# Performance work log

Measured on AMD Instinct MI355X. Metric: run time of the kernel, lower is better.

The kernel has to match this reference:

```python
import jax, jax.numpy as jnp
import numpy as np

B, S, E, F = 8, 1024, 1024, 4096
EPS = 1e-12

def _layer_norm(x, gamma, beta):
    mu = jnp.mean(x, axis=-1, keepdims=True)
    var = jnp.mean(jnp.square(x - mu), axis=-1, keepdims=True)
    return (x - mu) / jnp.sqrt(var + EPS) * gamma + beta

def setup_inputs() -> dict:
    key = jax.random.key(0)
    ks = jax.random.split(key, 16)
    sE = 1.0 / np.sqrt(E)
    sF = 1.0 / np.sqrt(F)
    return {
        'hidden_states': jax.random.normal(ks[0], (B, S, E), jnp.float32),
        'Wq': jax.random.normal(ks[1], (E, E), jnp.float32) * sE,
        'bq': jnp.zeros((E,), jnp.float32),
        'Wk': jax.random.normal(ks[2], (E, E), jnp.float32) * sE,
        'bk': jnp.zeros((E,), jnp.float32),
        'Wv': jax.random.normal(ks[3], (E, E), jnp.float32) * sE,
        'bv': jnp.zeros((E,), jnp.float32),
        'Wd': jax.random.normal(ks[4], (E, E), jnp.float32) * sE,
        'bd': jnp.zeros((E,), jnp.float32),
        'g1': jnp.ones((E,), jnp.float32),
        'b1': jnp.zeros((E,), jnp.float32),
        'Wi': jax.random.normal(ks[5], (E, F), jnp.float32) * sE,
        'bi': jnp.zeros((F,), jnp.float32),
        'Wo': jax.random.normal(ks[6], (F, E), jnp.float32) * sF,
        'bo': jnp.zeros((E,), jnp.float32),
        'g2': jnp.ones((E,), jnp.float32),
        'b2': jnp.zeros((E,), jnp.float32),
    }

def reference(hidden_states, Wq, bq, Wk, bk, Wv, bv, Wd, bd, g1, b1, Wi, bi, Wo, bo, g2, b2):
    x = hidden_states
    q = x @ Wq + bq                     # [B,S,E]
    k = x @ Wk + bk
    v = x @ Wv + bv
    scores = jnp.einsum('bqe,bke->bqk', q, k) / jnp.sqrt(jnp.float32(E))
    attn_w = jax.nn.softmax(scores, axis=-1)
    attn_out = jnp.einsum('bqk,bke->bqe', attn_w, v)
    # add_norm 1 (dropout = identity in eval)
    h1 = _layer_norm(attn_out @ Wd + bd + x, g1, b1)
    ff = jax.nn.gelu(h1 @ Wi + bi, approximate=False)   # forward_act
    # NOTE: original code's second add_norm uses forward_act (pre out_dense),
    # applying out_dense inside add_norm -> LN(out_dense(ff) + h1)
    out = _layer_norm(ff @ Wo + bo + h1, g2, b2)
    return out
```

## Files before the change

### kernel.cpp

```cpp
#include <hip/hip_runtime.h>
#include <math.h>


typedef __bf16 bf16;
typedef __attribute__((ext_vector_type(8))) __bf16 bf16x8;
typedef __attribute__((ext_vector_type(4))) __bf16 bf16x4;
typedef __attribute__((ext_vector_type(4))) float f32x4;

#define BM 128
#define BN 128
#define BK 64
#define SCS 140

__device__ __forceinline__ void async_cp16(const bf16* g, bf16* l) {
    __builtin_amdgcn_global_load_lds((__attribute__((address_space(1))) void*)(g),
                                     (__attribute__((address_space(3))) void*)(l),
                                     16, 0, 0);
}

__device__ __forceinline__ float gelu_fast(float x) {
    float u = x * x;
    float y = 1.5957691216f * x * fmaf(0.044715f, u, 1.0f);
    float e = __expf(-y);
    return x * __builtin_amdgcn_rcpf(1.0f + e);
}

__device__ __forceinline__ float load_dual(const void* p, long long i, int f32) {
    return f32 ? ((const float*)p)[i] : (float)((const bf16*)p)[i];
}


__global__ void diag_init(const void* x, int* dflag)
{
    const int t = threadIdx.x;
    const bf16* xb = (const bf16*)x;
    float a = (float)xb[2 * t];
    float b = (float)xb[2 * t + 1];
    auto wild = [](float v) -> bool {
        float af = fabsf(v);
        return !(af <= 3.0e38f) || af > 1.0e3f || (v != 0.0f && af < 1.0e-8f);
    };
    unsigned long long ba = __ballot(wild(a));
    unsigned long long bb = __ballot(wild(b));
    if (t == 0) *dflag = (__popcll(ba) + __popcll(bb) > 16) ? 1 : 0;
}

__global__ void sentinel_small(float* out) { out[0] = 2048.0f; }


__global__ __launch_bounds__(256)
void convert_vec4(const void* src, bf16* dst, long long n4, const int* dflag)
{
    const int f32 = *dflag;
    long long i = (long long)blockIdx.x * 256 + threadIdx.x;
    if (i >= n4) return;
    bf16x4 o;
    if (f32) {
        f32x4 v = ((const f32x4*)src)[i];
        #pragma unroll
        for (int j = 0; j < 4; j++) o[j] = (bf16)v[j];
    } else {
        o = ((const bf16x4*)src)[i];
    }
    ((bf16x4*)dst)[i] = o;
}

struct SmallPtrs { const void* p[10]; };

__global__ __launch_bounds__(256)
void convert_small(SmallPtrs sp, bf16* dst, const int* dflag)
{
    const int f32 = *dflag;
    const int idx = blockIdx.x * 256 + threadIdx.x;
    if (idx >= 13312) return;
    const int seg = idx >> 10;
    float v;
    if (seg < 9) v = load_dual(sp.p[seg], idx & 1023, f32);
    else         v = load_dual(sp.p[9], idx - 9216, f32);
    dst[idx] = (bf16)v;
}

__global__ __launch_bounds__(256)
void transpose_dual(const void* in, bf16* out, int R, int C, const int* dflag)
{
    __shared__ bf16 tile[32][33];
    const int f32 = *dflag;
    const int c0 = blockIdx.x * 32, r0 = blockIdx.y * 32;
    const int tx = threadIdx.x, ty = threadIdx.y;
    #pragma unroll
    for (int i = 0; i < 32; i += 8)
        tile[ty + i][tx] = (bf16)load_dual(in, (long long)(r0 + ty + i) * C + (c0 + tx), f32);
    __syncthreads();
    #pragma unroll
    for (int i = 0; i < 32; i += 8)
        out[(long long)(c0 + ty + i) * R + (r0 + tx)] = tile[tx][ty + i];
}

__global__ __launch_bounds__(256)
void transpose_b(const bf16* __restrict__ in, bf16* __restrict__ out, int R, int C)
{
    __shared__ bf16 tile[32][33];
    const long long z = (long long)blockIdx.z * (long long)R * C;
    const int c0 = blockIdx.x * 32, r0 = blockIdx.y * 32;
    const int tx = threadIdx.x, ty = threadIdx.y;
    #pragma unroll
    for (int i = 0; i < 32; i += 8)
        tile[ty + i][tx] = in[z + (long long)(r0 + ty + i) * C + (c0 + tx)];
    __syncthreads();
    #pragma unroll
    for (int i = 0; i < 32; i += 8)
        out[z + (long long)(c0 + ty + i) * R + (r0 + tx)] = tile[tx][ty + i];
}

template<int ACT, int HAS_BIAS, int HAS_RES, int OUT_F32>
__global__ __launch_bounds__(512)
void gemm_bt(const bf16* __restrict__ A, const bf16* __restrict__ Bt,
             const bf16* __restrict__ bias, const bf16* __restrict__ res,
             void* __restrict__ Cout, int M, int N, int K, float scale,
             long long bsA, long long bsB, long long bsC, long long bsBias)
{
    __shared__ __align__(16) char smem[65536];
    float* sC = (float*)smem;

    const int tid  = threadIdx.x;
    const int lane = tid & 63;
    const int wave = tid >> 6;
    const int pw   = wave & 3;
    const int wm   = pw >> 1;
    const int wn   = pw & 1;
    const bool producer = (wave >= 4);
    const int m0   = blockIdx.y * BM;
    const int n0   = blockIdx.x * BN;
    const long long zA = (long long)blockIdx.z * bsA;
    const long long zB = (long long)blockIdx.z * bsB;
    const long long zC = (long long)blockIdx.z * bsC;
    const bf16* biasz = HAS_BIAS ? (bias + (long long)blockIdx.z * bsBias) : nullptr;
    const int nIter = K >> 6;

    f32x4 acc[4][4];
    const bf16* gA[4]; const bf16* gB[4]; int lo[4];

    if (producer) {
        #pragma unroll
        for (int j = 0; j < 4; j++) {
            const int ci  = j * 256 + pw * 64 + lane;
            const int row = ci >> 3;
            const int c8  = ((ci & 7) ^ (row & 7)) * 8;
            gA[j] = A + zA + (long long)(m0 + row) * K + c8;
            gB[j] = Bt + zB + (long long)(n0 + row) * K + c8;
            lo[j] = (j * 256 + pw * 64) * 8;
        }
        bf16* dA = (bf16*)smem;
        bf16* dB = (bf16*)(smem + 16384);
        #pragma unroll
        for (int j = 0; j < 4; j++) {
            async_cp16(gA[j], dA + lo[j]);
            async_cp16(gB[j], dB + lo[j]);
            gA[j] += BK; gB[j] += BK;
        }
    } else {
        const f32x4 zf = {0.f, 0.f, 0.f, 0.f};
        #pragma unroll
        for (int i = 0; i < 4; i++)
            #pragma unroll
            for (int j = 0; j < 4; j++) acc[i][j] = zf;
    }
    __syncthreads();

    const int fr   = lane & 15;
    const int x0   = (lane >> 4) ^ (fr & 7);
    const int arow = wm * 64 + fr;
    const int brow = wn * 64 + fr;

    for (int kt = 0; kt < nIter; ++kt) {
        if (producer) {
            if (kt + 1 < nIter) {
                const int bo = ((kt + 1) & 1) ? 32768 : 0;
                bf16* dA = (bf16*)(smem + bo);
                bf16* dB = (bf16*)(smem + bo + 16384);
                #pragma unroll
                for (int j = 0; j < 4; j++) {
                    async_cp16(gA[j], dA + lo[j]);
                    async_cp16(gB[j], dB + lo[j]);
                    gA[j] += BK; gB[j] += BK;
                }
            }
        } else {
            const int bo = (kt & 1) ? 32768 : 0;
            const bf16* sAk = (const bf16*)(smem + bo);
            const bf16* sBk = (const bf16*)(smem + bo + 16384);
            #pragma unroll
            for (int s = 0; s < 2; s++) {
                const int xo = (x0 ^ (s << 2)) * 8;
                bf16x8 afr[4], bfr[4];
                #pragma unroll
                for (int mi = 0; mi < 4; mi++) afr[mi] = *(const bf16x8*)(sAk + (arow + mi * 16) * 64 + xo);
                #pragma unroll
                for (int ni = 0; ni < 4; ni++) bfr[ni] = *(const bf16x8*)(sBk + (brow + ni * 16) * 64 + xo);
                #pragma unroll
                for (int mi = 0; mi < 4; mi++)
                    #pragma unroll
                    for (int ni = 0; ni < 4; ni++)
                        acc[mi][ni] = __builtin_amdgcn_mfma_f32_16x16x32_bf16(afr[mi], bfr[ni], acc[mi][ni], 0, 0, 0);
            }
        }
        __syncthreads();
    }

    const int q4 = lane >> 4;
    for (int h = 0; h < 2; h++) {
        __syncthreads();
        if (!producer && wm == h) {
            #pragma unroll
            for (int mi = 0; mi < 4; mi++)
                #pragma unroll
                for (int r = 0; r < 4; r++) {
                    const int lr = mi * 16 + q4 * 4 + r;
                    #pragma unroll
                    for (int ni = 0; ni < 4; ni++)
                        sC[lr * SCS + wn * 64 + ni * 16 + fr] = acc[mi][ni][r];
                }
        }
        __syncthreads();
        const int lr = tid >> 3;
        const int cb = (tid & 7) * 16;
        const long long grow  = m0 + h * 64 + lr;
        const long long gbase = zC + grow * (long long)N + (n0 + cb);
        const float* srow = sC + lr * SCS + cb;
        #pragma unroll
        for (int g = 0; g < 2; g++) {
            f32x4 v0 = *(const f32x4*)(srow + g * 8);
            f32x4 v1 = *(const f32x4*)(srow + g * 8 + 4);
            float vv[8] = {v0[0], v0[1], v0[2], v0[3], v1[0], v1[1], v1[2], v1[3]};
            if constexpr (HAS_BIAS) {
                bf16x8 bb = *(const bf16x8*)(biasz + n0 + cb + g * 8);
                #pragma unroll
                for (int j = 0; j < 8; j++) vv[j] = vv[j] * scale + (float)bb[j];
            } else {
                #pragma unroll
                for (int j = 0; j < 8; j++) vv[j] *= scale;
            }
            if constexpr (ACT == 1) {
                #pragma unroll
                for (int j = 0; j < 8; j++) vv[j] = gelu_fast(vv[j]);
            }
            if constexpr (HAS_RES) {
                bf16x8 rr = *(const bf16x8*)(res + gbase + g * 8);
                #pragma unroll
                for (int j = 0; j < 8; j++) vv[j] += (float)rr[j];
            }
            if constexpr (OUT_F32) {
                f32x4 o0 = {vv[0], vv[1], vv[2], vv[3]};
                f32x4 o1 = {vv[4], vv[5], vv[6], vv[7]};
                *(f32x4*)((float*)Cout + gbase + g * 8)     = o0;
                *(f32x4*)((float*)Cout + gbase + g * 8 + 4) = o1;
            } else {
                bf16x8 o;
                #pragma unroll
                for (int j = 0; j < 8; j++) o[j] = (bf16)vv[j];
                *(bf16x8*)((bf16*)Cout + gbase + g * 8) = o;
            }
        }
    }
}


__global__ __launch_bounds__(256)
void softmax_inplace(bf16* __restrict__ P, int N)
{
    const long long row = blockIdx.x;
    bf16* p = P + row * (long long)N;
    const int t = threadIdx.x;
    bf16x4 xin = *(const bf16x4*)(p + t * 4);
    float xs[4];
    #pragma unroll
    for (int i = 0; i < 4; i++) xs[i] = (float)xin[i];

    float m = fmaxf(fmaxf(xs[0], xs[1]), fmaxf(xs[2], xs[3]));
    #pragma unroll
    for (int off = 32; off > 0; off >>= 1) m = fmaxf(m, __shfl_xor(m, off, 64));
    __shared__ float red[4];
    if ((t & 63) == 0) red[t >> 6] = m;
    __syncthreads();
    m = fmaxf(fmaxf(red[0], red[1]), fmaxf(red[2], red[3]));

    float e[4], s = 0.f;
    #pragma unroll
    for (int i = 0; i < 4; i++) { e[i] = __expf(xs[i] - m); s += e[i]; }
    #pragma unroll
    for (int off = 32; off > 0; off >>= 1) s += __shfl_xor(s, off, 64);
    __shared__ float red2[4];
    if ((t & 63) == 0) red2[t >> 6] = s;
    __syncthreads();
    s = red2[0] + red2[1] + red2[2] + red2[3];
    const float inv = 1.f / s;

    bf16x4 o;
    #pragma unroll
    for (int i = 0; i < 4; i++) o[i] = (bf16)(e[i] * inv);
    *(bf16x4*)(p + t * 4) = o;
}

template<int IN_F32, int OUT_F32>
__global__ __launch_bounds__(256)
void layernorm_rows(const void* __restrict__ Z, const bf16* __restrict__ g,
                    const bf16* __restrict__ b, void* __restrict__ outp, int N)
{
    const long long row = blockIdx.x;
    const int t = threadIdx.x;
    float xv[4];
    if constexpr (IN_F32) {
        f32x4 zin = *(const f32x4*)((const float*)Z + row * (long long)N + t * 4);
        #pragma unroll
        for (int i = 0; i < 4; i++) xv[i] = zin[i];
    } else {
        bf16x4 zin = *(const bf16x4*)((const bf16*)Z + row * (long long)N + t * 4);
        #pragma unroll
        for (int i = 0; i < 4; i++) xv[i] = (float)zin[i];
    }

    float s = xv[0] + xv[1] + xv[2] + xv[3];
    #pragma unroll
    for (int off = 32; off > 0; off >>= 1) s += __shfl_xor(s, off, 64);
    __shared__ float r1[4];
    if ((t & 63) == 0) r1[t >> 6] = s;
    __syncthreads();
    const float mu = (r1[0] + r1[1] + r1[2] + r1[3]) * (1.f / 1024.f);

    float d[4];
    float sq = 0.f;
    #pragma unroll
    for (int i = 0; i < 4; i++) { d[i] = xv[i] - mu; sq += d[i] * d[i]; }
    #pragma unroll
    for (int off = 32; off > 0; off >>= 1) sq += __shfl_xor(sq, off, 64);
    __shared__ float r2[4];
    if ((t & 63) == 0) r2[t >> 6] = sq;
    __syncthreads();
    const float var = (r2[0] + r2[1] + r2[2] + r2[3]) * (1.f / 1024.f);
    const float rstd = rsqrtf(var + 1e-12f);

    bf16x4 gv = *(const bf16x4*)(g + t * 4);
    bf16x4 bv = *(const bf16x4*)(b + t * 4);
    if constexpr (OUT_F32) {
        f32x4 o;
        #pragma unroll
        for (int i = 0; i < 4; i++)
            o[i] = d[i] * rstd * (float)gv[i] + (float)bv[i];
        *(f32x4*)((float*)outp + row * (long long)N + t * 4) = o;
    } else {
        bf16x4 o;
        #pragma unroll
        for (int i = 0; i < 4; i++)
            o[i] = (bf16)(d[i] * rstd * (float)gv[i] + (float)bv[i]);
        *(bf16x4*)((bf16*)outp + row * (long long)N + t * 4) = o;
    }
}


extern "C" void kernel_launch(void* const* d_in, const int* in_sizes, int n_in,
                              void* d_out, int out_size, void* d_ws, size_t ws_size,
                              hipStream_t stream)
{
    (void)in_sizes; (void)n_in; (void)out_size;

    const void* x  = d_in[0];
    const void* Wq = d_in[1];  const void* bq = d_in[2];
    const void* Wk = d_in[3];  const void* bk = d_in[4];
    const void* Wv = d_in[5];  const void* bv = d_in[6];
    const void* Wd = d_in[7];  const void* bd = d_in[8];
    const void* g1 = d_in[9];  const void* b1 = d_in[10];
    const void* Wi = d_in[11]; const void* bi = d_in[12];
    const void* Wo = d_in[13]; const void* bo = d_in[14];
    const void* g2 = d_in[15]; const void* b2 = d_in[16];

    const int Bb = 8, S = 1024, E = 1024, F = 4096;
    const int M = Bb * S;
    const long long SE = (long long)S * E, SS = (long long)S * S;
    const long long ME = (long long)M * E;

    char* ws = (char*)d_ws;
    const size_t MB = 1024ull * 1024ull;
    int*  dflag = (int*)(ws + 0);
    bf16* small = (bf16*)(ws + 64 * 1024);
    bf16* bq_c = small + 0 * 1024;
    bf16* bd_c = small + 3 * 1024;
    bf16* g1_c = small + 4 * 1024;
    bf16* b1_c = small + 5 * 1024;
    bf16* g2_c = small + 6 * 1024;
    bf16* b2_c = small + 7 * 1024;
    bf16* bo_c = small + 8 * 1024;
    bf16* bi_c = small + 9216;
    bf16* WoT  = (bf16*)(ws + 1 * MB);
    bf16* WiT  = (bf16*)(ws + 9 * MB);
    bf16* WqT  = (bf16*)(ws + 17 * MB);
    bf16* WkT  = (bf16*)(ws + 19 * MB);
    bf16* WvT  = (bf16*)(ws + 21 * MB);
    bf16* WdT  = (bf16*)(ws + 23 * MB);
    bf16* xb   = (bf16*)(ws + 25 * MB);
    float* out = (float*)d_out;

    diag_init<<<1, 64, 0, stream>>>(x, dflag);

    if (ws_size < 70 * MB) { sentinel_small<<<1, 1, 0, stream>>>(out); return; }

    SmallPtrs sp;
    sp.p[0] = bq; sp.p[1] = bk; sp.p[2] = bv; sp.p[3] = bd; sp.p[4] = g1;
    sp.p[5] = b1; sp.p[6] = g2; sp.p[7] = b2; sp.p[8] = bo; sp.p[9] = bi;
    convert_small<<<52, 256, 0, stream>>>(sp, small, dflag);
    convert_vec4<<<8192, 256, 0, stream>>>(x, xb, ME / 4, dflag);

    const dim3 tb(32, 8, 1);
    transpose_dual<<<dim3(E/32, E/32), tb, 0, stream>>>(Wq, WqT, E, E, dflag);
    transpose_dual<<<dim3(E/32, E/32), tb, 0, stream>>>(Wk, WkT, E, E, dflag);
    transpose_dual<<<dim3(E/32, E/32), tb, 0, stream>>>(Wv, WvT, E, E, dflag);
    transpose_dual<<<dim3(E/32, E/32), tb, 0, stream>>>(Wd, WdT, E, E, dflag);
    transpose_dual<<<dim3(F/32, E/32), tb, 0, stream>>>(Wi, WiT, E, F, dflag);
    transpose_dual<<<dim3(E/32, F/32), tb, 0, stream>>>(Wo, WoT, F, E, dflag);

    if (ws_size >= 121 * MB) {
        bf16* qkv  = (bf16*)(ws + 41 * MB);
        bf16* q    = qkv;
        bf16* k    = qkv + ME;
        bf16* v    = qkv + 2 * ME;
        bf16* vT   = (bf16*)(ws + 89 * MB);
        bf16* P    = (bf16*)(ws + 73 * MB);
        bf16* attn = (bf16*)(ws + 41 * MB);
        bf16* z1   = (bf16*)(ws + 57 * MB);
        bf16* h1   = (bf16*)(ws + 41 * MB);
        bf16* ff   = (bf16*)(ws + 57 * MB);
        float* z2f = (float*)(ws + 9 * MB);

        gemm_bt<0,1,0,0><<<dim3(8, 64, 3), 512, 0, stream>>>(
            xb, WqT, bq_c, nullptr, qkv, M, E, E, 1.f, 0, (long long)E * E, ME, E);
        transpose_b<<<dim3(E/32, S/32, Bb), tb, 0, stream>>>(v, vT, S, E);
        gemm_bt<0,0,0,0><<<dim3(8, 8, Bb), 512, 0, stream>>>(
            q, k, nullptr, nullptr, P, S, S, E, 0.03125f, SE, SE, SS, 0);
        softmax_inplace<<<M, 256, 0, stream>>>(P, S);
        gemm_bt<0,0,0,0><<<dim3(8, 8, Bb), 512, 0, stream>>>(
            P, vT, nullptr, nullptr, attn, S, E, S, 1.f, SS, SE, SE, 0);
        gemm_bt<0,1,1,0><<<dim3(8, 64), 512, 0, stream>>>(
            attn, WdT, bd_c, xb, z1, M, E, E, 1.f, 0, 0, 0, 0);
        layernorm_rows<0,0><<<M, 256, 0, stream>>>(z1, g1_c, b1_c, h1, E);
        gemm_bt<1,1,0,0><<<dim3(32, 64), 512, 0, stream>>>(
            h1, WiT, bi_c, nullptr, ff, M, F, E, 1.f, 0, 0, 0, 0);
        gemm_bt<0,1,1,1><<<dim3(8, 64), 512, 0, stream>>>(
            ff, WoT, bo_c, h1, z2f, M, E, F, 1.f, 0, 0, 0, 0);
        layernorm_rows<1,1><<<M, 256, 0, stream>>>(z2f, g2_c, b2_c, out, E);
    } else {
        bf16* qkv_b = (bf16*)(ws + 41 * MB);
        bf16* q_b   = qkv_b;
        bf16* k_b   = qkv_b + SE;
        bf16* v_b   = qkv_b + 2 * SE;
        bf16* vT_b  = (bf16*)(ws + 47 * MB);
        bf16* P_b   = (bf16*)(ws + 49 * MB);
        bf16* at_b  = (bf16*)(ws + 51 * MB);
        bf16* z1_b  = (bf16*)(ws + 53 * MB);
        bf16* h1_b  = (bf16*)(ws + 55 * MB);
        bf16* ff_b  = (bf16*)(ws + 57 * MB);
        bf16* z2_b  = (bf16*)(ws + 65 * MB);

        for (int b = 0; b < Bb; b++) {
            const bf16* x_b = xb + (long long)b * SE;
            gemm_bt<0,1,0,0><<<dim3(8, 8, 3), 512, 0, stream>>>(
                x_b, WqT, bq_c, nullptr, qkv_b, S, E, E, 1.f, 0, (long long)E * E, SE, E);
            transpose_b<<<dim3(E/32, S/32), tb, 0, stream>>>(v_b, vT_b, S, E);
            gemm_bt<0,0,0,0><<<dim3(8, 8), 512, 0, stream>>>(
                q_b, k_b, nullptr, nullptr, P_b, S, S, E, 0.03125f, 0, 0, 0, 0);
            softmax_inplace<<<S, 256, 0, stream>>>(P_b, S);
            gemm_bt<0,0,0,0><<<dim3(8, 8), 512, 0, stream>>>(
                P_b, vT_b, nullptr, nullptr, at_b, S, E, S, 1.f, 0, 0, 0, 0);
            gemm_bt<0,1,1,0><<<dim3(8, 8), 512, 0, stream>>>(
                at_b, WdT, bd_c, x_b, z1_b, S, E, E, 1.f, 0, 0, 0, 0);
            layernorm_rows<0,0><<<S, 256, 0, stream>>>(z1_b, g1_c, b1_c, h1_b, E);
            gemm_bt<1,1,0,0><<<dim3(32, 8), 512, 0, stream>>>(
                h1_b, WiT, bi_c, nullptr, ff_b, S, F, E, 1.f, 0, 0, 0, 0);
            gemm_bt<0,1,1,0><<<dim3(8, 8), 512, 0, stream>>>(
                ff_b, WoT, bo_c, h1_b, z2_b, S, E, F, 1.f, 0, 0, 0, 0);
            layernorm_rows<0,1><<<S, 256, 0, stream>>>(z2_b, g2_c, b2_c, out + (long long)b * SE, E);
        }
    }
}
```

Baseline: 532.3 us.

## Add 256x256 pipelined GEMM with XCD remap and split-K for dense projections

Introduces a new 256x256-tile bf16 MFMA GEMM kernel. It uses a 128KB double-buffered LDS, async global-to-LDS loads, a hand-scheduled phase pipeline with barriers and setprio, and workgroup remapping across XCDs. The new kernel replaces the QKV projection and both FFN GEMMs. The output GEMM uses 2-way split-K into two fp32 buffers, and the final layernorm now sums both. The goal is higher data reuse and MFMA utilization on the large GEMMs, at the cost of extra fp32 traffic for the split-K partials and lower occupancy from the large LDS footprint.

```diff
diff --git a/kernel.cpp b/kernel.cpp
--- a/kernel.cpp
+++ b/kernel.cpp
@@ -264,6 +264,196 @@
     }
 }
 
+template<int ACT, int HAS_BIAS, int HAS_RES, int OUT_F32, int SPLITK>
+__global__ __launch_bounds__(512, 2)
+void gemm256(const bf16* __restrict__ A, const bf16* __restrict__ Bt,
+             const bf16* __restrict__ bias, const bf16* __restrict__ res,
+             void* __restrict__ Cout, void* __restrict__ Cout2,
+             int M, int N, int K, int ldk, float scale,
+             long long bsB, long long bsC, long long bsBias)
+{
+    __shared__ __align__(16) char smem[131072];
+
+    const int tid  = threadIdx.x;
+    const int lane = tid & 63;
+    const int wave = tid >> 6;
+    const int wm   = wave >> 2;
+    const int wn   = wave & 3;
+
+    const int gx  = N >> 8;
+    const int nwg = gx * (M >> 8);
+    int wg = blockIdx.x;
+    {
+        const int q = nwg >> 3, r = nwg & 7;
+        const int xcd = wg & 7, lid = wg >> 3;
+        wg = (xcd < r ? xcd * (q + 1) : r * (q + 1) + (xcd - r) * q) + lid;
+    }
+    const int bx = wg % gx, by = wg / gx;
+    const int m0 = by << 8, n0 = bx << 8;
+    const int zi = blockIdx.y;
+
+    const bf16* Ab = A  + (SPLITK ? (long long)zi * K : 0);
+    const bf16* Bb = Bt + (SPLITK ? (long long)zi * K : (long long)zi * bsB);
+    const bool  bon = HAS_BIAS && (!SPLITK || zi == 0);
+    const bool  ron = HAS_RES  && (!SPLITK || zi == 0);
+    const bf16* biasz = HAS_BIAS ? (bias + (SPLITK ? 0 : (long long)zi * bsBias)) : nullptr;
+    const long long coff = SPLITK ? 0 : (long long)zi * bsC;
+    char* const Cb = (char*)((SPLITK && zi) ? Cout2 : Cout);
+
+    int soff[2];
+    #pragma unroll
+    for (int qq = 0; qq < 2; qq++) {
+        const int g   = (wave * 2 + qq) * 64 + lane;
+        const int rp  = g >> 3, sub = g & 7;
+        const int row = rp * 2 + (sub >> 2);
+        const int cc  = (sub & 3) ^ (rp & 3);
+        soff[qq] = row * ldk + cc * 8;
+    }
+    const bf16* aS0 = Ab + (long long)m0 * ldk + soff[0];
+    const bf16* aS1 = Ab + (long long)m0 * ldk + soff[1];
+    const bf16* bS0 = Bb + (long long)n0 * ldk + soff[0];
+    const bf16* bS1 = Bb + (long long)n0 * ldk + soff[1];
+    char* const ldsW = smem + wave * 2048;
+
+    const int fr = lane & 15, chk = lane >> 4;
+    const int ra  = wm * 128 + fr;
+    const int aRd = (ra >> 1) * 128 + (ra & 1) * 64 + ((chk ^ ((ra >> 1) & 3)) * 16);
+    const int rb  = wn * 64 + fr;
+    const int bRd = 32768 + (rb >> 1) * 128 + (rb & 1) * 64 + ((chk ^ ((rb >> 1) & 3)) * 16);
+
+#define STG(buf, mat, h, t) do { \
+    char* _d = ldsW + (buf) * 65536 + (mat) * 32768 + (h) * 16384; \
+    const int _ko = (t) * 64 + (h) * 32; \
+    async_cp16(((mat) ? bS0 : aS0) + _ko, (bf16*)_d); \
+    async_cp16(((mat) ? bS1 : aS1) + _ko, (bf16*)(_d + 1024)); \
+} while (0)
+#define IF_STG(c, buf, mat, h, t) do { if (c) STG(buf, mat, h, t); } while (0)
+#define NO_WAIT do {} while (0)
+#define VM_WAIT(c) do { \
+    if (c) asm volatile("s_waitcnt vmcnt(6)" ::: "memory"); \
+    else   asm volatile("s_waitcnt vmcnt(0)" ::: "memory"); \
+} while (0)
+#define PHASE(cbuf, s, mh, DOB, STAGE_STMT, WAIT_STMT) do { \
+    bf16x8 av[4]; \
+    _Pragma("unroll") \
+    for (int _i = 0; _i < 4; _i++) \
+        av[_i] = *(const bf16x8*)(smem + (cbuf) * 65536 + (s) * 16384 + ((mh) * 4 + _i) * 1024 + aRd); \
+    if (DOB) { \
+        _Pragma("unroll") \
+        for (int _j = 0; _j < 4; _j++) \
+            bv[_j] = *(const bf16x8*)(smem + (cbuf) * 65536 + (s) * 16384 + _j * 1024 + bRd); \
+    } \
+    STAGE_STMT; \
+    asm volatile("s_barrier" ::: "memory"); \
+    asm volatile("s_waitcnt lgkmcnt(0)" ::: "memory"); \
+    __builtin_amdgcn_sched_barrier(0); \
+    __builtin_amdgcn_s_setprio(1); \
+    _Pragma("unroll") \
+    for (int _i = 0; _i < 4; _i++) \
+        _Pragma("unroll") \
+        for (int _j = 0; _j < 4; _j++) \
+            acc[(mh) * 4 + _i][_j] = __builtin_amdgcn_mfma_f32_16x16x32_bf16(av[_i], bv[_j], acc[(mh) * 4 + _i][_j], 0, 0, 0); \
+    __builtin_amdgcn_s_setprio(0); \
+    WAIT_STMT; \
+    asm volatile("s_barrier" ::: "memory"); \
+} while (0)
+
+    const int NT = K >> 6, NI = NT >> 1;
+
+    STG(0, 1, 0, 0); STG(0, 0, 0, 0); STG(0, 1, 1, 0); STG(0, 0, 1, 0);
+    STG(1, 1, 0, 1); STG(1, 0, 0, 1); STG(1, 1, 1, 1);
+
+    f32x4 acc[8][4];
+    {
+        const f32x4 zf = {0.f, 0.f, 0.f, 0.f};
+        #pragma unroll
+        for (int i = 0; i < 8; i++)
+            #pragma unroll
+            for (int j = 0; j < 4; j++) acc[i][j] = zf;
+    }
+    bf16x8 bv[4];
+
+    asm volatile("s_waitcnt vmcnt(6)" ::: "memory");
+    asm volatile("s_barrier" ::: "memory");
+
+    for (int it = 0; it < NI; ++it) {
+        const int o = 2 * it + 1, e2 = 2 * it + 2, o2 = 2 * it + 3;
+        const bool se = e2 < NT, so = o2 < NT;
+        PHASE(0, 0, 0, 1, STG(1, 0, 1, o),          NO_WAIT);
+        PHASE(0, 0, 1, 0, IF_STG(se, 0, 1, 0, e2),  NO_WAIT);
+        PHASE(0, 1, 0, 1, IF_STG(se, 0, 0, 0, e2),  NO_WAIT);
+        PHASE(0, 1, 1, 0, IF_STG(se, 0, 1, 1, e2),  VM_WAIT(se));
+        PHASE(1, 0, 0, 1, IF_STG(se, 0, 0, 1, e2),  NO_WAIT);
+        PHASE(1, 0, 1, 0, IF_STG(so, 1, 1, 0, o2),  NO_WAIT);
+        PHASE(1, 1, 0, 1, IF_STG(so, 1, 0, 0, o2),  NO_WAIT);
+        PHASE(1, 1, 1, 0, IF_STG(so, 1, 1, 1, o2),  VM_WAIT(so));
+    }
+#undef PHASE
+#undef VM_WAIT
+#undef NO_WAIT
+#undef IF_STG
+#undef STG
+
+    float* sC = (float*)smem;
+    const int q4 = lane >> 4;
+    const int lr = tid >> 3;
+    const int c0 = (tid & 7) * 4;
+    const long long Nll = N;
+    #pragma unroll
+    for (int p = 0; p < 4; p++) {
+        __syncthreads();
+        if (wm == (p >> 1)) {
+            #pragma unroll
+            for (int i = 0; i < 4; i++) {
+                const int fi = (p & 1) * 4 + i;
+                #pragma unroll
+                for (int r = 0; r < 4; r++) {
+                    const int row = i * 16 + q4 * 4 + r;
+                    #pragma unroll
+                    for (int j = 0; j < 4; j++)
+                        sC[row * 260 + wn * 64 + j * 16 + fr] = acc[fi][j][r];
+                }
+            }
+        }
+        __syncthreads();
+        const long long grow = m0 + p * 64 + lr;
+        const long long gb = grow * Nll + n0;
+        const float* srow = sC + lr * 260;
+        #pragma unroll
+        for (int g = 0; g < 8; g++) {
+            const int col = c0 + g * 32;
+            f32x4 v = *(const f32x4*)(srow + col);
+            float vv[4] = {v[0], v[1], v[2], v[3]};
+            if (bon) {
+                bf16x4 bb = *(const bf16x4*)(biasz + n0 + col);
+                #pragma unroll
+                for (int j = 0; j < 4; j++) vv[j] = vv[j] * scale + (float)bb[j];
+            } else {
+                #pragma unroll
+                for (int j = 0; j < 4; j++) vv[j] *= scale;
+            }
+            if constexpr (ACT == 1) {
+                #pragma unroll
+                for (int j = 0; j < 4; j++) vv[j] = gelu_fast(vv[j]);
+            }
+            if (ron) {
+                bf16x4 rr = *(const bf16x4*)(res + gb + col);
+                #pragma unroll
+                for (int j = 0; j < 4; j++) vv[j] += (float)rr[j];
+            }
+            if constexpr (OUT_F32) {
+                f32x4 o4 = {vv[0], vv[1], vv[2], vv[3]};
+                *(f32x4*)((float*)Cb + coff + gb + col) = o4;
+            } else {
+                bf16x4 o4;
+                #pragma unroll
+                for (int j = 0; j < 4; j++) o4[j] = (bf16)vv[j];
+                *(bf16x4*)((bf16*)Cb + coff + gb + col) = o4;
+            }
+        }
+    }
+}
+
 
 __global__ __launch_bounds__(256)
 void softmax_inplace(bf16* __restrict__ P, int N)
@@ -301,18 +491,24 @@
     *(bf16x4*)(p + t * 4) = o;
 }
 
-template<int IN_F32, int OUT_F32>
+template<int IN_MODE, int OUT_F32>
 __global__ __launch_bounds__(256)
-void layernorm_rows(const void* __restrict__ Z, const bf16* __restrict__ g,
-                    const bf16* __restrict__ b, void* __restrict__ outp, int N)
+void layernorm_rows(const void* __restrict__ Z, const void* __restrict__ Z2,
+                    const bf16* __restrict__ g, const bf16* __restrict__ b,
+                    void* __restrict__ outp, int N)
 {
     const long long row = blockIdx.x;
     const int t = threadIdx.x;
     float xv[4];
-    if constexpr (IN_F32) {
+    if constexpr (IN_MODE >= 1) {
         f32x4 zin = *(const f32x4*)((const float*)Z + row * (long long)N + t * 4);
         #pragma unroll
         for (int i = 0; i < 4; i++) xv[i] = zin[i];
+        if constexpr (IN_MODE == 2) {
+            f32x4 z2 = *(const f32x4*)((const float*)Z2 + row * (long long)N + t * 4);
+            #pragma unroll
+            for (int i = 0; i < 4; i++) xv[i] += z2[i];
+        }
     } else {
         bf16x4 zin = *(const bf16x4*)((const bf16*)Z + row * (long long)N + t * 4);
         #pragma unroll
@@ -428,10 +624,12 @@
         bf16* z1   = (bf16*)(ws + 57 * MB);
         bf16* h1   = (bf16*)(ws + 41 * MB);
         bf16* ff   = (bf16*)(ws + 57 * MB);
-        float* z2f = (float*)(ws + 9 * MB);
-
-        gemm_bt<0,1,0,0><<<dim3(8, 64, 3), 512, 0, stream>>>(
-            xb, WqT, bq_c, nullptr, qkv, M, E, E, 1.f, 0, (long long)E * E, ME, E);
+        float* z2a = (float*)(ws + 9 * MB);
+        float* z2b = (float*)(ws + 89 * MB);
+
+        gemm256<0,1,0,0,0><<<dim3((E/256)*(M/256), 3), 512, 0, stream>>>(
+            xb, WqT, bq_c, nullptr, qkv, nullptr, M, E, E, E, 1.f,
+            (long long)E * E, ME, E);
         transpose_b<<<dim3(E/32, S/32, Bb), tb, 0, stream>>>(v, vT, S, E);
         gemm_bt<0,0,0,0><<<dim3(8, 8, Bb), 512, 0, stream>>>(
             q, k, nullptr, nullptr, P, S, S, E, 0.03125f, SE, SE, SS, 0);
@@ -440,12 +638,12 @@
             P, vT, nullptr, nullptr, attn, S, E, S, 1.f, SS, SE, SE, 0);
         gemm_bt<0,1,1,0><<<dim3(8, 64), 512, 0, stream>>>(
             attn, WdT, bd_c, xb, z1, M, E, E, 1.f, 0, 0, 0, 0);
-        layernorm_rows<0,0><<<M, 256, 0, stream>>>(z1, g1_c, b1_c, h1, E);
-        gemm_bt<1,1,0,0><<<dim3(32, 64), 512, 0, stream>>>(
-            h1, WiT, bi_c, nullptr, ff, M, F, E, 1.f, 0, 0, 0, 0);
-        gemm_bt<0,1,1,1><<<dim3(8, 64), 512, 0, stream>>>(
-            ff, WoT, bo_c, h1, z2f, M, E, F, 1.f, 0, 0, 0, 0);
-        layernorm_rows<1,1><<<M, 256, 0, stream>>>(z2f, g2_c, b2_c, out, E);
+        layernorm_rows<0,0><<<M, 256, 0, stream>>>(z1, nullptr, g1_c, b1_c, h1, E);
+        gemm256<1,1,0,0,0><<<dim3((F/256)*(M/256), 1), 512, 0, stream>>>(
+            h1, WiT, bi_c, nullptr, ff, nullptr, M, F, E, E, 1.f, 0, 0, 0);
+        gemm256<0,1,1,1,1><<<dim3((E/256)*(M/256), 2), 512, 0, stream>>>(
+            ff, WoT, bo_c, h1, z2a, z2b, M, E, F / 2, F, 1.f, 0, 0, 0);
+        layernorm_rows<2,1><<<M, 256, 0, stream>>>(z2a, z2b, g2_c, b2_c, out, E);
     } else {
         bf16* qkv_b = (bf16*)(ws + 41 * MB);
         bf16* q_b   = qkv_b;
@@ -471,12 +669,12 @@
                 P_b, vT_b, nullptr, nullptr, at_b, S, E, S, 1.f, 0, 0, 0, 0);
             gemm_bt<0,1,1,0><<<dim3(8, 8), 512, 0, stream>>>(
                 at_b, WdT, bd_c, x_b, z1_b, S, E, E, 1.f, 0, 0, 0, 0);
-            layernorm_rows<0,0><<<S, 256, 0, stream>>>(z1_b, g1_c, b1_c, h1_b, E);
+            layernorm_rows<0,0><<<S, 256, 0, stream>>>(z1_b, nullptr, g1_c, b1_c, h1_b, E);
             gemm_bt<1,1,0,0><<<dim3(32, 8), 512, 0, stream>>>(
                 h1_b, WiT, bi_c, nullptr, ff_b, S, F, E, 1.f, 0, 0, 0, 0);
             gemm_bt<0,1,1,0><<<dim3(8, 8), 512, 0, stream>>>(
                 ff_b, WoT, bo_c, h1_b, z2_b, S, E, F, 1.f, 0, 0, 0, 0);
-            layernorm_rows<0,1><<<S, 256, 0, stream>>>(z2_b, g2_c, b2_c, out + (long long)b * SE, E);
-        }
-    }
-}
+            layernorm_rows<0,1><<<S, 256, 0, stream>>>(z2_b, nullptr, g2_c, b2_c, out + (long long)b * SE, E);
+        }
+    }
+}
```

After: 507.1 us. 4.7% less time.
